# Performance work log

Measured on AMD Instinct MI355X. Metric: run time of the kernel, lower is better.

The kernel has to match this reference:

```python
import jax, jax.numpy as jnp
import numpy as np

N_CLASSES = 64  # number of initial (labeled) classes


def _compute_logits_radii(h, protos, radii):
    """Complex-valued radii logits.
    h: [B,N,2,D] (real/imag), protos: [B,2,C,D], radii: [B,C].
    dist[b,n,c] = sum_d (hr-pr)^2 + (hi-pi)^2 (matches _compute_distances_complex).
    logits = -dist / (2*radii)  (standard IMP radii-logit form).
    Expanded as |h|^2 + |p|^2 - 2 h.p so the cross term is a GEMM (no [N,C,D] tensor).
    """
    hr, hi = h[:, :, 0, :], h[:, :, 1, :]          # [B,N,D]
    pr, pi = protos[:, 0], protos[:, 1]            # [B,C,D]
    h_sq = jnp.sum(hr * hr + hi * hi, axis=-1)     # [B,N]
    p_sq = jnp.sum(pr * pr + pi * pi, axis=-1)     # [B,C]
    cross = jnp.einsum('bnd,bcd->bnc', hr, pr) + jnp.einsum('bnd,bcd->bnc', hi, pi)
    dist = h_sq[:, :, None] + p_sq[:, None, :] - 2.0 * cross   # [B,N,C]
    return -dist / (2.0 * radii[:, None, :])


def setup_inputs() -> dict:
    key = jax.random.key(0)
    k1, k2, k3, k4, k5 = jax.random.split(key, 5)
    B, N, C, D = 1, 8192, 512, 512
    h = jax.random.normal(k1, (B, N, 2, D), dtype=jnp.float32)
    protos = jax.random.normal(k2, (B, 2, C, D), dtype=jnp.float32)
    # radii must be positive (it divides the distance); keep away from 0
    radii = jax.random.uniform(k3, (B, C), dtype=jnp.float32) * 0.9 + 0.1
    y = jax.random.randint(k4, (N,), 0, N_CLASSES)
    support_labels = jax.random.randint(k5, (C,), 0, N_CLASSES)
    return {"h": h, "protos": protos, "radii": radii, "y": y,
            "support_labels": support_labels, "n_initial_clusters": N_CLASSES}


def reference(h, protos, radii, y, support_labels, n_initial_clusters):
    logits = _compute_logits_radii(h, protos, radii)[0]          # [N,C], B=1 squeeze
    labels = jnp.where(y >= n_initial_clusters, -1, y)           # [N]
    support_targets = labels[:, None] == support_labels[None, :]  # [N,C] bool

    neg_inf = jnp.asarray(-jnp.inf, logits.dtype)
    # best prototype among the query's own class ('or' target)
    target_logits = jnp.where(support_targets, logits, neg_inf)
    best_targets = jnp.argmax(target_logits, axis=1)             # [N]

    # vectorized per-class best prototype: weights[n,c]=1 iff c is the argmax
    # of logits[n,:] restricted to clusters whose label == support_labels[c]
    max_per_class = jax.ops.segment_max(logits.T, support_labels,
                                        num_segments=N_CLASSES)  # [K,N]
    weights = (logits == max_per_class[support_labels, :].T).astype(logits.dtype)  # [N,C]

    # weighted cross entropy at the 'or' target
    log_probs = jax.nn.log_softmax(logits, axis=1)
    nll = -jnp.take_along_axis(log_probs, best_targets[:, None], axis=1)[:, 0]
    w = jnp.take_along_axis(weights, best_targets[:, None], axis=1)[:, 0]
    loss = jnp.mean(nll * w)

    # accuracy: predicted cluster -> its class label
    support_preds = jnp.argmax(logits, axis=1)
    y_pred = support_labels[support_preds]
    acc_val = jnp.sum((y_pred == labels).astype(jnp.float32))
    return loss, acc_val
```

## Files before the change

kernel.cpp:

```cpp
#include <hip/hip_runtime.h>
#include <stdint.h>

typedef unsigned short u16;
typedef __attribute__((ext_vector_type(8))) short shortx8;
typedef __attribute__((ext_vector_type(4))) float floatx4;

#define N_ROWS 8192
#define N_COLS 512
#define KDIM   1024

__device__ __forceinline__ u16 f2bf(float f) {
    union { float f; uint32_t u; } x; x.f = f;
    uint32_t u = x.u;
    uint32_t r = (u + 0x7FFFu + ((u >> 16) & 1u)) >> 16;
    return (u16)r;
}

__device__ __forceinline__ void async_copy16(const void* g, void* l) {
    __builtin_amdgcn_global_load_lds(
        (const __attribute__((address_space(1))) void*)g,
        (__attribute__((address_space(3))) void*)l, 16, 0, 0);
}

__global__ __launch_bounds__(256) void conv_hp(const float* __restrict__ h,
                                               const float* __restrict__ protos,
                                               u16* __restrict__ hb,
                                               u16* __restrict__ bb,
                                               float* __restrict__ hsq,
                                               float* __restrict__ psq,
                                               float* __restrict__ out) {
    int t = threadIdx.x, lane = t & 63, w = t >> 6;
    int bid = blockIdx.x;
    if (bid == 0 && t == 0) { out[0] = 0.0f; out[1] = 0.0f; }
    if (bid < 512) {
        int wave = bid * 4 + w;
        for (int q = 0; q < 4; q++) {
            int row = wave * 4 + q;
            const float4* src = (const float4*)(h + (size_t)row * KDIM);
            ushort4* dst = (ushort4*)(hb + (size_t)row * KDIM);
            float s = 0.0f;
            #pragma unroll
            for (int j = 0; j < 4; j++) {
                float4 v = src[lane + j * 64];
                s += v.x * v.x + v.y * v.y + v.z * v.z + v.w * v.w;
                dst[lane + j * 64] = make_ushort4(f2bf(v.x), f2bf(v.y), f2bf(v.z), f2bf(v.w));
            }
            #pragma unroll
            for (int off = 32; off; off >>= 1) s += __shfl_xor(s, off);
            if (lane == 0) hsq[row] = s;
        }
    } else {
        int c = (bid - 512) * 4 + w;
        const float4* pr = (const float4*)(protos + (size_t)c * 512);
        const float4* pi = (const float4*)(protos + 512 * 512 + (size_t)c * 512);
        ushort4* dr = (ushort4*)(bb + (size_t)c * KDIM);
        ushort4* di = (ushort4*)(bb + (size_t)c * KDIM + 512);
        float s = 0.0f;
        #pragma unroll
        for (int j = 0; j < 2; j++) {
            float4 a = pr[lane + j * 64];
            float4 b = pi[lane + j * 64];
            s += a.x * a.x + a.y * a.y + a.z * a.z + a.w * a.w;
            s += b.x * b.x + b.y * b.y + b.z * b.z + b.w * b.w;
            dr[lane + j * 64] = make_ushort4(f2bf(a.x), f2bf(a.y), f2bf(a.z), f2bf(a.w));
            di[lane + j * 64] = make_ushort4(f2bf(b.x), f2bf(b.y), f2bf(b.z), f2bf(b.w));
        }
        #pragma unroll
        for (int off = 32; off; off >>= 1) s += __shfl_xor(s, off);
        if (lane == 0) psq[c] = s;
    }
}

__global__ __launch_bounds__(256) void gemm_partials(const u16* __restrict__ hb,
                                                     const u16* __restrict__ bb,
                                                     const float* __restrict__ hsq,
                                                     const float* __restrict__ psq,
                                                     const float* __restrict__ radii,
                                                     const int* __restrict__ y,
                                                     const int* __restrict__ slab,
                                                     const int* __restrict__ ninit_p,
                                                     float* __restrict__ pmax_g,
                                                     int* __restrict__ pidx_g,
                                                     float* __restrict__ prmax_g,
                                                     float* __restrict__ pc0_g,
                                                     float* __restrict__ psum_g,
                                                     float* __restrict__ l0arr) {
    constexpr int BM = 128, BN = 64, BK = 64;
    __shared__ __align__(16) u16 As[BM * BK];
    __shared__ __align__(16) u16 Bs[BN * BK];
    __shared__ float smax[2][128];
    __shared__ int   scol[2][128];
    __shared__ float srmx[2][128];
    __shared__ float sc0v[2][128];
    __shared__ float ssum[2][128];

    int t = threadIdx.x, lane = t & 63, w = t >> 6;
    int wr = (w & 1) * 64;
    int wc = (w >> 1) * 32;

    int bid = blockIdx.x;
    int xcd = bid & 7;
    int idin = bid >> 3;
    int bx = (xcd << 3) | (idin >> 3);
    int by = idin & 7;
    int bm0 = bx * BM;
    int bn0 = by * BN;

    int tr = t >> 3, tc = t & 7;
    const u16* gA[4]; u16* lA[4];
    #pragma unroll
    for (int i = 0; i < 4; i++) {
        int row = tr + 32 * i;
        int kc = tc ^ (row & 7);
        gA[i] = hb + (size_t)(bm0 + row) * KDIM + kc * 8;
        lA[i] = &As[(t + 256 * i) * 8];
    }
    const u16* gB[2]; u16* lB[2];
    #pragma unroll
    for (int i = 0; i < 2; i++) {
        int row = tr + 32 * i;
        int kc = tc ^ (row & 7);
        gB[i] = bb + (size_t)(bn0 + row) * KDIM + kc * 8;
        lB[i] = &Bs[(t + 256 * i) * 8];
    }

    floatx4 acc[4][2] = {};

    int kq = lane >> 4, l7 = lane & 7, m = lane & 15;
    int swz0 = ((kq) ^ l7) * 8;
    int swz1 = ((4 + kq) ^ l7) * 8;
    const u16* paA = &As[(wr + m) * BK];
    const u16* paB = &Bs[(wc + m) * BK];

    for (int k0 = 0; k0 < KDIM; k0 += BK) {
        __syncthreads();
        #pragma unroll
        for (int i = 0; i < 4; i++) async_copy16(gA[i], lA[i]);
        #pragma unroll
        for (int i = 0; i < 2; i++) async_copy16(gB[i], lB[i]);
        #pragma unroll
        for (int i = 0; i < 4; i++) gA[i] += BK;
        #pragma unroll
        for (int i = 0; i < 2; i++) gB[i] += BK;
        __syncthreads();

        #pragma unroll
        for (int s = 0; s < 2; s++) {
            int sw = s ? swz1 : swz0;
            shortx8 af[4], bf[2];
            #pragma unroll
            for (int i = 0; i < 4; i++) af[i] = *(const shortx8*)(paA + i * 16 * BK + sw);
            #pragma unroll
            for (int j = 0; j < 2; j++) bf[j] = *(const shortx8*)(paB + j * 16 * BK + sw);
            #pragma unroll
            for (int i = 0; i < 4; i++)
                #pragma unroll
                for (int j = 0; j < 2; j++)
                    acc[i][j] = __builtin_amdgcn_mfma_f32_16x16x32_bf16(af[i], bf[j], acc[i][j], 0, 0, 0);
        }
    }

    int c0 = bn0 + wc + m, c1 = c0 + 16;
    float ps0 = psq[c0], ps1 = psq[c1];
    float inv0 = 0.5f / radii[c0], inv1 = 0.5f / radii[c1];
    int sl0 = slab[c0], sl1 = slab[c1];
    int slabz = slab[0];
    int ninit = ninit_p[0];
    int ch = w >> 1;
    bool isL0 = (bn0 == 0) && (wc == 0) && (m == 0);

    #pragma unroll
    for (int i = 0; i < 4; i++) {
        #pragma unroll
        for (int r = 0; r < 4; r++) {
            int n = bm0 + wr + i * 16 + kq * 4 + r;
            float hsqn = hsq[n];
            int yv = y[n];
            int lab = (yv >= ninit) ? -1 : yv;
            float v0 = (2.0f * acc[i][0][r] - hsqn - ps0) * inv0;
            float v1 = (2.0f * acc[i][1][r] - hsqn - ps1) * inv1;
            if (isL0) l0arr[n] = v0;

            float bmax = v0; int bcol = c0;
            if (v1 > bmax) { bmax = v1; bcol = c1; }
            float brm = -INFINITY;
            if (sl0 == lab) brm = v0;
            if (sl1 == lab && v1 > brm) brm = v1;
            float bc0 = -INFINITY;
            if (sl0 == slabz) bc0 = v0;
            if (sl1 == slabz && v1 > bc0) bc0 = v1;
            #pragma unroll
            for (int off = 1; off < 16; off <<= 1) {
                float ov = __shfl_xor(bmax, off); int oc = __shfl_xor(bcol, off);
                if (ov > bmax || (ov == bmax && oc < bcol)) { bmax = ov; bcol = oc; }
                float orv = __shfl_xor(brm, off); if (orv > brm) brm = orv;
                float oc0 = __shfl_xor(bc0, off); if (oc0 > bc0) bc0 = oc0;
            }
            float se = __expf(v0 - bmax) + __expf(v1 - bmax);
            #pragma unroll
            for (int off = 1; off < 16; off <<= 1) se += __shfl_xor(se, off);
            if (m == 0) {
                int rl = (w & 1) * 64 + i * 16 + kq * 4 + r;
                smax[ch][rl] = bmax; scol[ch][rl] = bcol;
                srmx[ch][rl] = brm;  sc0v[ch][rl] = bc0; ssum[ch][rl] = se;
            }
        }
    }
    __syncthreads();
    if (t < 128) {
        int n = bm0 + t;
        size_t gi_ = (size_t)by * N_ROWS + n;
        float m0 = smax[0][t], m1 = smax[1][t];
        int i0 = scol[0][t], i1 = scol[1][t];
        float gm; int gi;
        if (m0 > m1 || (m0 == m1 && i0 < i1)) { gm = m0; gi = i0; }
        else { gm = m1; gi = i1; }
        pmax_g[gi_] = gm;
        pidx_g[gi_] = gi;
        prmax_g[gi_] = fmaxf(srmx[0][t], srmx[1][t]);
        pc0_g[gi_]  = fmaxf(sc0v[0][t], sc0v[1][t]);
        psum_g[gi_] = ssum[0][t] * __expf(m0 - gm) + ssum[1][t] * __expf(m1 - gm);
    }
}

__global__ __launch_bounds__(256) void combine(const float* __restrict__ pmax_g,
                                               const int* __restrict__ pidx_g,
                                               const float* __restrict__ prmax_g,
                                               const float* __restrict__ pc0_g,
                                               const float* __restrict__ psum_g,
                                               const float* __restrict__ l0arr,
                                               const int* __restrict__ y,
                                               const int* __restrict__ slab,
                                               const int* __restrict__ ninit_p,
                                               float* __restrict__ out) {
    int t = threadIdx.x, lane = t & 63, w = t >> 6;
    int n = blockIdx.x * 256 + t;

    float gm = -INFINITY; int gi = 0x7fffffff;
    float rm = -INFINITY, c0m = -INFINITY;
    float pm[8];
    #pragma unroll
    for (int cb = 0; cb < 8; cb++) {
        size_t idx = (size_t)cb * N_ROWS + n;
        float p = pmax_g[idx]; int pi = pidx_g[idx];
        pm[cb] = p;
        if (p > gm || (p == gm && pi < gi)) { gm = p; gi = pi; }
        rm = fmaxf(rm, prmax_g[idx]);
        c0m = fmaxf(c0m, pc0_g[idx]);
    }
    float den = 0.0f;
    #pragma unroll
    for (int cb = 0; cb < 8; cb++)
        den += psum_g[(size_t)cb * N_ROWS + n] * __expf(pm[cb] - gm);
    float lse = gm + __logf(den);

    int yv = y[n];
    int lab = (yv >= ninit_p[0]) ? -1 : yv;
    float nll, wgt;
    if (rm != -INFINITY) { nll = lse - rm; wgt = 1.0f; }
    else {
        float l0 = l0arr[n];
        nll = lse - l0;
        wgt = (l0 == c0m) ? 1.0f : 0.0f;
    }
    int ypred = slab[gi];
    float li = nll * wgt * (1.0f / (float)N_ROWS);
    float ai = (ypred == lab) ? 1.0f : 0.0f;

    #pragma unroll
    for (int off = 32; off; off >>= 1) {
        li += __shfl_xor(li, off);
        ai += __shfl_xor(ai, off);
    }
    __shared__ float pl[4], pa_[4];
    if (lane == 0) { pl[w] = li; pa_[w] = ai; }
    __syncthreads();
    if (t == 0) {
        atomicAdd(&out[0], pl[0] + pl[1] + pl[2] + pl[3]);
        atomicAdd(&out[1], pa_[0] + pa_[1] + pa_[2] + pa_[3]);
    }
}

extern "C" void kernel_launch(void* const* d_in, const int* in_sizes, int n_in,
                              void* d_out, int out_size, void* d_ws, size_t ws_size,
                              hipStream_t stream) {
    const float* h      = (const float*)d_in[0];
    const float* protos = (const float*)d_in[1];
    const float* radii  = (const float*)d_in[2];
    const int*   y      = (const int*)d_in[3];
    const int*   slab   = (const int*)d_in[4];
    const int*   ninit  = (const int*)d_in[5];
    float* out = (float*)d_out;

    char* ws = (char*)d_ws;
    u16*   hb    = (u16*)(ws);
    u16*   bb    = (u16*)(ws + 16777216);
    float* hsq   = (float*)(ws + 17825792);
    float* psq   = (float*)(ws + 17858560);
    float* pmax  = (float*)(ws + 17860608);
    int*   pidx  = (int*)  (ws + 18122752);
    float* prmax = (float*)(ws + 18384896);
    float* pc0   = (float*)(ws + 18647040);
    float* psum  = (float*)(ws + 18909184);
    float* l0arr = (float*)(ws + 19171328);

    conv_hp<<<640, 256, 0, stream>>>(h, protos, hb, bb, hsq, psq, out);
    gemm_partials<<<512, 256, 0, stream>>>(hb, bb, hsq, psq, radii, y, slab, ninit,
                                           pmax, pidx, prmax, pc0, psum, l0arr);
    combine<<<N_ROWS / 256, 256, 0, stream>>>(pmax, pidx, prmax, pc0, psum,
                                              l0arr, y, slab, ninit, out);
}
```

Baseline: 117.8 us.

## Fuse h fp32-to-bf16 conversion and norm into GEMM A-tile loading

Removes the separate pass that converted h to a bf16 workspace and computed row norms. The GEMM now reads fp32 h directly into registers, accumulates the squared norm, converts to bf16 with the hardware intrinsic, and writes the swizzled A tile to LDS. The prototype B tile is double-buffered with async copies. This drops a 32MB read plus 16MB write round trip, but every one of the 8 column-tile blocks now re-reads fp32 h (twice the bytes of bf16) and does the conversion redundantly. The A loads are register-prefetched rather than async.

Measured after the change: 140.0 us. 1.19x slower.

```diff
diff --git a/kernel.cpp b/kernel.cpp
--- a/kernel.cpp
+++ b/kernel.cpp
@@ -1,4 +1,5 @@
 #include <hip/hip_runtime.h>
+#include <hip/hip_bf16.h>
 #include <stdint.h>
 
 typedef unsigned short u16;
@@ -16,78 +17,61 @@
     return (u16)r;
 }
 
+__device__ __forceinline__ u16 f2bf_hw(float f) {
+    union { __hip_bfloat16 b; u16 u; } x;
+    x.b = __float2bfloat16(f);
+    return x.u;
+}
+
 __device__ __forceinline__ void async_copy16(const void* g, void* l) {
     __builtin_amdgcn_global_load_lds(
         (const __attribute__((address_space(1))) void*)g,
         (__attribute__((address_space(3))) void*)l, 16, 0, 0);
 }
 
-__global__ __launch_bounds__(256) void conv_hp(const float* __restrict__ h,
-                                               const float* __restrict__ protos,
-                                               u16* __restrict__ hb,
-                                               u16* __restrict__ bb,
-                                               float* __restrict__ hsq,
-                                               float* __restrict__ psq,
-                                               float* __restrict__ out) {
+__global__ __launch_bounds__(256) void prep(const float* __restrict__ protos,
+                                            u16* __restrict__ bb,
+                                            float* __restrict__ psq,
+                                            float* __restrict__ out) {
     int t = threadIdx.x, lane = t & 63, w = t >> 6;
-    int bid = blockIdx.x;
-    if (bid == 0 && t == 0) { out[0] = 0.0f; out[1] = 0.0f; }
-    if (bid < 512) {
-        int wave = bid * 4 + w;
-        for (int q = 0; q < 4; q++) {
-            int row = wave * 4 + q;
-            const float4* src = (const float4*)(h + (size_t)row * KDIM);
-            ushort4* dst = (ushort4*)(hb + (size_t)row * KDIM);
-            float s = 0.0f;
-            #pragma unroll
-            for (int j = 0; j < 4; j++) {
-                float4 v = src[lane + j * 64];
-                s += v.x * v.x + v.y * v.y + v.z * v.z + v.w * v.w;
-                dst[lane + j * 64] = make_ushort4(f2bf(v.x), f2bf(v.y), f2bf(v.z), f2bf(v.w));
-            }
-            #pragma unroll
-            for (int off = 32; off; off >>= 1) s += __shfl_xor(s, off);
-            if (lane == 0) hsq[row] = s;
-        }
-    } else {
-        int c = (bid - 512) * 4 + w;
-        const float4* pr = (const float4*)(protos + (size_t)c * 512);
-        const float4* pi = (const float4*)(protos + 512 * 512 + (size_t)c * 512);
-        ushort4* dr = (ushort4*)(bb + (size_t)c * KDIM);
-        ushort4* di = (ushort4*)(bb + (size_t)c * KDIM + 512);
-        float s = 0.0f;
-        #pragma unroll
-        for (int j = 0; j < 2; j++) {
-            float4 a = pr[lane + j * 64];
-            float4 b = pi[lane + j * 64];
-            s += a.x * a.x + a.y * a.y + a.z * a.z + a.w * a.w;
-            s += b.x * b.x + b.y * b.y + b.z * b.z + b.w * b.w;
-            dr[lane + j * 64] = make_ushort4(f2bf(a.x), f2bf(a.y), f2bf(a.z), f2bf(a.w));
-            di[lane + j * 64] = make_ushort4(f2bf(b.x), f2bf(b.y), f2bf(b.z), f2bf(b.w));
-        }
-        #pragma unroll
-        for (int off = 32; off; off >>= 1) s += __shfl_xor(s, off);
-        if (lane == 0) psq[c] = s;
-    }
-}
-
-__global__ __launch_bounds__(256) void gemm_partials(const u16* __restrict__ hb,
-                                                     const u16* __restrict__ bb,
-                                                     const float* __restrict__ hsq,
-                                                     const float* __restrict__ psq,
-                                                     const float* __restrict__ radii,
-                                                     const int* __restrict__ y,
-                                                     const int* __restrict__ slab,
-                                                     const int* __restrict__ ninit_p,
-                                                     float* __restrict__ pmax_g,
-                                                     int* __restrict__ pidx_g,
-                                                     float* __restrict__ prmax_g,
-                                                     float* __restrict__ pc0_g,
-                                                     float* __restrict__ psum_g,
-                                                     float* __restrict__ l0arr) {
-    constexpr int BM = 128, BN = 64, BK = 64;
+    if (blockIdx.x == 0 && t == 0) { out[0] = 0.0f; out[1] = 0.0f; }
+    int c = blockIdx.x * 4 + w;
+    const float4* pr = (const float4*)(protos + (size_t)c * 512);
+    const float4* pi = (const float4*)(protos + 512 * 512 + (size_t)c * 512);
+    ushort4* dr = (ushort4*)(bb + (size_t)c * KDIM);
+    ushort4* di = (ushort4*)(bb + (size_t)c * KDIM + 512);
+    float s = 0.0f;
+    #pragma unroll
+    for (int j = 0; j < 2; j++) {
+        float4 a = pr[lane + j * 64];
+        float4 b = pi[lane + j * 64];
+        s += a.x * a.x + a.y * a.y + a.z * a.z + a.w * a.w;
+        s += b.x * b.x + b.y * b.y + b.z * b.z + b.w * b.w;
+        dr[lane + j * 64] = make_ushort4(f2bf(a.x), f2bf(a.y), f2bf(a.z), f2bf(a.w));
+        di[lane + j * 64] = make_ushort4(f2bf(b.x), f2bf(b.y), f2bf(b.z), f2bf(b.w));
+    }
+    #pragma unroll
+    for (int off = 32; off; off >>= 1) s += __shfl_xor(s, off);
+    if (lane == 0) psq[c] = s;
+}
+
+__global__ __launch_bounds__(256) void gemm_fused(const float* __restrict__ h,
+                                                  const u16* __restrict__ bb,
+                                                  const float* __restrict__ psq,
+                                                  const float* __restrict__ radii,
+                                                  const int* __restrict__ y,
+                                                  const int* __restrict__ slab,
+                                                  const int* __restrict__ ninit_p,
+                                                  float* __restrict__ pmax_g,
+                                                  int* __restrict__ pidx_g,
+                                                  float* __restrict__ prmax_g,
+                                                  float* __restrict__ pc0_g,
+                                                  float* __restrict__ psum_g,
+                                                  float* __restrict__ l0arr) {
+    constexpr int BM = 128, BN = 64, BK = 64, NSTEP = KDIM / BK;
     __shared__ __align__(16) u16 As[BM * BK];
-    __shared__ __align__(16) u16 Bs[BN * BK];
+    __shared__ __align__(16) u16 Bs[2][BN * BK];
+    __shared__ float shsq[BM];
     __shared__ float smax[2][128];
     __shared__ int   scol[2][128];
     __shared__ float srmx[2][128];
@@ -106,44 +90,64 @@
     int bm0 = bx * BM;
     int bn0 = by * BN;
 
+    int arow = t >> 1, ahalf = t & 1;
+    const float4* gA = (const float4*)(h + (size_t)(bm0 + arow) * KDIM + ahalf * 32);
+    u16* lAw[4];
+    #pragma unroll
+    for (int j = 0; j < 4; j++) {
+        int kcg = ahalf * 4 + j;
+        lAw[j] = &As[arow * BK + ((kcg ^ (arow & 7)) * 8)];
+    }
+
     int tr = t >> 3, tc = t & 7;
-    const u16* gA[4]; u16* lA[4];
-    #pragma unroll
-    for (int i = 0; i < 4; i++) {
-        int row = tr + 32 * i;
-        int kc = tc ^ (row & 7);
-        gA[i] = hb + (size_t)(bm0 + row) * KDIM + kc * 8;
-        lA[i] = &As[(t + 256 * i) * 8];
-    }
-    const u16* gB[2]; u16* lB[2];
+    const u16* gB[2];
+    int lBoff[2];
     #pragma unroll
     for (int i = 0; i < 2; i++) {
         int row = tr + 32 * i;
         int kc = tc ^ (row & 7);
         gB[i] = bb + (size_t)(bn0 + row) * KDIM + kc * 8;
-        lB[i] = &Bs[(t + 256 * i) * 8];
+        lBoff[i] = (t + 256 * i) * 8;
     }
 
     floatx4 acc[4][2] = {};
-
     int kq = lane >> 4, l7 = lane & 7, m = lane & 15;
     int swz0 = ((kq) ^ l7) * 8;
     int swz1 = ((4 + kq) ^ l7) * 8;
     const u16* paA = &As[(wr + m) * BK];
-    const u16* paB = &Bs[(wc + m) * BK];
-
-    for (int k0 = 0; k0 < KDIM; k0 += BK) {
+
+    float hs = 0.0f;
+    float4 av[8];
+
+    #pragma unroll
+    for (int j = 0; j < 8; j++) av[j] = gA[j];
+    #pragma unroll
+    for (int i = 0; i < 2; i++) async_copy16(gB[i], &Bs[0][lBoff[i]]);
+
+    for (int step = 0; step < NSTEP; ++step) {
         __syncthreads();
         #pragma unroll
-        for (int i = 0; i < 4; i++) async_copy16(gA[i], lA[i]);
-        #pragma unroll
-        for (int i = 0; i < 2; i++) async_copy16(gB[i], lB[i]);
-        #pragma unroll
-        for (int i = 0; i < 4; i++) gA[i] += BK;
-        #pragma unroll
-        for (int i = 0; i < 2; i++) gB[i] += BK;
+        for (int j = 0; j < 4; j++) {
+            float4 a = av[2 * j], b = av[2 * j + 1];
+            hs += a.x * a.x + a.y * a.y + a.z * a.z + a.w * a.w
+                + b.x * b.x + b.y * b.y + b.z * b.z + b.w * b.w;
+            shortx8 p;
+            p[0] = (short)f2bf_hw(a.x); p[1] = (short)f2bf_hw(a.y);
+            p[2] = (short)f2bf_hw(a.z); p[3] = (short)f2bf_hw(a.w);
+            p[4] = (short)f2bf_hw(b.x); p[5] = (short)f2bf_hw(b.y);
+            p[6] = (short)f2bf_hw(b.z); p[7] = (short)f2bf_hw(b.w);
+            *(shortx8*)lAw[j] = p;
+        }
         __syncthreads();
-
+        if (step + 1 < NSTEP) {
+            const float4* gAn = gA + (step + 1) * 16;
+            #pragma unroll
+            for (int j = 0; j < 8; j++) av[j] = gAn[j];
+            #pragma unroll
+            for (int i = 0; i < 2; i++)
+                async_copy16(gB[i] + (size_t)(step + 1) * BK, &Bs[(step + 1) & 1][lBoff[i]]);
+        }
+        const u16* paB = &Bs[step & 1][(wc + m) * BK];
         #pragma unroll
         for (int s = 0; s < 2; s++) {
             int sw = s ? swz1 : swz0;
@@ -151,14 +155,18 @@
             #pragma unroll
             for (int i = 0; i < 4; i++) af[i] = *(const shortx8*)(paA + i * 16 * BK + sw);
             #pragma unroll
-            for (int j = 0; j < 2; j++) bf[j] = *(const shortx8*)(paB + j * 16 * BK + sw);
+            for (int jj = 0; jj < 2; jj++) bf[jj] = *(const shortx8*)(paB + jj * 16 * BK + sw);
             #pragma unroll
             for (int i = 0; i < 4; i++)
                 #pragma unroll
-                for (int j = 0; j < 2; j++)
-                    acc[i][j] = __builtin_amdgcn_mfma_f32_16x16x32_bf16(af[i], bf[j], acc[i][j], 0, 0, 0);
+                for (int jj = 0; jj < 2; jj++)
+                    acc[i][jj] = __builtin_amdgcn_mfma_f32_16x16x32_bf16(af[i], bf[jj], acc[i][jj], 0, 0, 0);
         }
     }
+
+    hs += __shfl_xor(hs, 1);
+    if (ahalf == 0) shsq[arow] = hs;
+    __syncthreads();
 
     int c0 = bn0 + wc + m, c1 = c0 + 16;
     float ps0 = psq[c0], ps1 = psq[c1];
@@ -173,8 +181,9 @@
     for (int i = 0; i < 4; i++) {
         #pragma unroll
         for (int r = 0; r < 4; r++) {
-            int n = bm0 + wr + i * 16 + kq * 4 + r;
-            float hsqn = hsq[n];
+            int lr = wr + i * 16 + kq * 4 + r;
+            int n = bm0 + lr;
+            float hsqn = shsq[lr];
             int yv = y[n];
             int lab = (yv >= ninit) ? -1 : yv;
             float v0 = (2.0f * acc[i][0][r] - hsqn - ps0) * inv0;
@@ -293,20 +302,18 @@
     float* out = (float*)d_out;
 
     char* ws = (char*)d_ws;
-    u16*   hb    = (u16*)(ws);
     u16*   bb    = (u16*)(ws + 16777216);
-    float* hsq   = (float*)(ws + 17825792);
-    float* psq   = (float*)(ws + 17858560);
     float* pmax  = (float*)(ws + 17860608);
     int*   pidx  = (int*)  (ws + 18122752);
     float* prmax = (float*)(ws + 18384896);
     float* pc0   = (float*)(ws + 18647040);
     float* psum  = (float*)(ws + 18909184);
     float* l0arr = (float*)(ws + 19171328);
-
-    conv_hp<<<640, 256, 0, stream>>>(h, protos, hb, bb, hsq, psq, out);
-    gemm_partials<<<512, 256, 0, stream>>>(hb, bb, hsq, psq, radii, y, slab, ninit,
-                                           pmax, pidx, prmax, pc0, psum, l0arr);
+    float* psq   = (float*)(ws + 17858560);
+
+    prep<<<128, 256, 0, stream>>>(protos, bb, psq, out);
+    gemm_fused<<<512, 256, 0, stream>>>(h, bb, psq, radii, y, slab, ninit,
+                                        pmax, pidx, prmax, pc0, psum, l0arr);
     combine<<<N_ROWS / 256, 256, 0, stream>>>(pmax, pidx, prmax, pc0, psum,
                                               l0arr, y, slab, ninit, out);
 }
```

## Double-buffer LDS tiles in the GEMM main loop to overlap loads with MFMA

Applied to the files above, without the earlier changes.

Splits the A and B shared-memory tiles into two buffers. The next K-step's async global-to-LDS copies are issued before the MFMAs run on the current buffer, and a single barrier closes each step instead of two. The K loop is also fully unrolled. The aim is to hide global load latency behind matrix math, at the cost of twice the LDS per block, which may reduce occupancy, and a larger code footprint.

Result: no change. 120.0 us (+1.8%).

```diff
diff --git a/kernel.cpp b/kernel.cpp
--- a/kernel.cpp
+++ b/kernel.cpp
@@ -85,9 +85,9 @@
                                                      float* __restrict__ pc0_g,
                                                      float* __restrict__ psum_g,
                                                      float* __restrict__ l0arr) {
-    constexpr int BM = 128, BN = 64, BK = 64;
-    __shared__ __align__(16) u16 As[BM * BK];
-    __shared__ __align__(16) u16 Bs[BN * BK];
+    constexpr int BM = 128, BN = 64, BK = 64, NSTEP = KDIM / BK;
+    __shared__ __align__(16) u16 As[2][BM * BK];
+    __shared__ __align__(16) u16 Bs[2][BN * BK];
     __shared__ float smax[2][128];
     __shared__ int   scol[2][128];
     __shared__ float srmx[2][128];
@@ -107,43 +107,57 @@
     int bn0 = by * BN;
 
     int tr = t >> 3, tc = t & 7;
-    const u16* gA[4]; u16* lA[4];
+    const u16* gA[4]; int lAoff[4];
     #pragma unroll
     for (int i = 0; i < 4; i++) {
         int row = tr + 32 * i;
         int kc = tc ^ (row & 7);
         gA[i] = hb + (size_t)(bm0 + row) * KDIM + kc * 8;
-        lA[i] = &As[(t + 256 * i) * 8];
-    }
-    const u16* gB[2]; u16* lB[2];
+        lAoff[i] = (t + 256 * i) * 8;
+    }
+    const u16* gB[2]; int lBoff[2];
     #pragma unroll
     for (int i = 0; i < 2; i++) {
         int row = tr + 32 * i;
         int kc = tc ^ (row & 7);
         gB[i] = bb + (size_t)(bn0 + row) * KDIM + kc * 8;
-        lB[i] = &Bs[(t + 256 * i) * 8];
+        lBoff[i] = (t + 256 * i) * 8;
     }
 
     floatx4 acc[4][2] = {};
-
     int kq = lane >> 4, l7 = lane & 7, m = lane & 15;
     int swz0 = ((kq) ^ l7) * 8;
     int swz1 = ((4 + kq) ^ l7) * 8;
-    const u16* paA = &As[(wr + m) * BK];
-    const u16* paB = &Bs[(wc + m) * BK];
-
-    for (int k0 = 0; k0 < KDIM; k0 += BK) {
-        __syncthreads();
-        #pragma unroll
-        for (int i = 0; i < 4; i++) async_copy16(gA[i], lA[i]);
-        #pragma unroll
-        for (int i = 0; i < 2; i++) async_copy16(gB[i], lB[i]);
-        #pragma unroll
-        for (int i = 0; i < 4; i++) gA[i] += BK;
-        #pragma unroll
-        for (int i = 0; i < 2; i++) gB[i] += BK;
-        __syncthreads();
-
+    int aro = (wr + m) * BK;
+    int bro = (wc + m) * BK;
+
+    #pragma unroll
+    for (int i = 0; i < 4; i++) async_copy16(gA[i], &As[0][lAoff[i]]);
+    #pragma unroll
+    for (int i = 0; i < 2; i++) async_copy16(gB[i], &Bs[0][lBoff[i]]);
+    #pragma unroll
+    for (int i = 0; i < 4; i++) gA[i] += BK;
+    #pragma unroll
+    for (int i = 0; i < 2; i++) gB[i] += BK;
+    __syncthreads();
+
+    #pragma unroll
+    for (int step = 0; step < NSTEP; ++step) {
+        int cur = step & 1;
+        if (step + 1 < NSTEP) {
+            #pragma unroll
+            for (int i = 0; i < 4; i++) {
+                async_copy16(gA[i], &As[cur ^ 1][lAoff[i]]);
+                gA[i] += BK;
+            }
+            #pragma unroll
+            for (int i = 0; i < 2; i++) {
+                async_copy16(gB[i], &Bs[cur ^ 1][lBoff[i]]);
+                gB[i] += BK;
+            }
+        }
+        const u16* paA = &As[cur][aro];
+        const u16* paB = &Bs[cur][bro];
         #pragma unroll
         for (int s = 0; s < 2; s++) {
             int sw = s ? swz1 : swz0;
@@ -151,13 +165,14 @@
             #pragma unroll
             for (int i = 0; i < 4; i++) af[i] = *(const shortx8*)(paA + i * 16 * BK + sw);
             #pragma unroll
-            for (int j = 0; j < 2; j++) bf[j] = *(const shortx8*)(paB + j * 16 * BK + sw);
+            for (int jj = 0; jj < 2; jj++) bf[jj] = *(const shortx8*)(paB + jj * 16 * BK + sw);
             #pragma unroll
             for (int i = 0; i < 4; i++)
                 #pragma unroll
-                for (int j = 0; j < 2; j++)
-                    acc[i][j] = __builtin_amdgcn_mfma_f32_16x16x32_bf16(af[i], bf[j], acc[i][j], 0, 0, 0);
-        }
+                for (int jj = 0; jj < 2; jj++)
+                    acc[i][jj] = __builtin_amdgcn_mfma_f32_16x16x32_bf16(af[i], bf[jj], acc[i][jj], 0, 0, 0);
+        }
+        __syncthreads();
     }
 
     int c0 = bn0 + wc + m, c1 = c0 + 16;
```
